# Performance work log

Hardware: AMD Instinct MI355X
Metric: run time of the kernel (lower is better)

The kernel has to match this reference:

```python
import jax, jax.numpy as jnp
import numpy as np

B, N = 32, 256
PHI1, PHI2 = 64, 128
RHO1, RHO2, OUT = 256, 128, 64


def setup_inputs() -> dict:
    key = jax.random.key(0)
    ks = jax.random.split(key, 12)
    dm = jax.random.normal(ks[0], (B, N, N), dtype=jnp.float32)
    lengths = jnp.clip(jax.random.randint(ks[1], (B,), 0, N), 2, N).astype(jnp.int32)

    def lin(k, fan_in, fan_out):
        # torch nn.Linear default init: U(-1/sqrt(fan_in), 1/sqrt(fan_in))
        bound = 1.0 / np.sqrt(fan_in)
        kw, kb = jax.random.split(k)
        W = jax.random.uniform(kw, (fan_in, fan_out), jnp.float32, -bound, bound)
        b = jax.random.uniform(kb, (fan_out,), jnp.float32, -bound, bound)
        return W, b

    W1, b1 = lin(ks[2], 1, PHI1)
    W2, b2 = lin(ks[3], PHI1, PHI2)
    W3, b3 = lin(ks[4], PHI2, RHO1)
    W4, b4 = lin(ks[5], RHO1, RHO2)
    W5, b5 = lin(ks[6], RHO2, OUT)
    return {"dm": dm, "lengths": lengths, "W1": W1, "b1": b1, "W2": W2, "b2": b2,
            "W3": W3, "b3": b3, "W4": W4, "b4": b4, "W5": W5, "b5": b5}


def reference(dm, lengths, W1, b1, W2, b2, W3, b3, W4, b4, W5, b5):
    # Static upper-triangular (offset=1) index pairs: P = N*(N-1)/2
    iu0, iu1 = jnp.triu_indices(N, k=1)
    scalars = dm[:, iu0, iu1]                                   # [B, P]
    # Ragged mask: a pair (i, j) exists only if both indices < item length
    mask = (iu0[None, :] < lengths[:, None]) & (iu1[None, :] < lengths[:, None])  # [B, P]
    # phi MLP applied per scalar: 1 -> 64 -> 128, ReLU after each
    h = jax.nn.relu(scalars[..., None] * W1[0] + b1)            # [B, P, 64]
    h = jax.nn.relu(jnp.einsum('bpd,de->bpe', h, W2) + b2)      # [B, P, 128]
    # Masked sum-pool over pairs
    pooled = jnp.sum(h * mask[..., None].astype(h.dtype), axis=1)  # [B, 128]
    # rho MLP: 128 -> 256 -> 128 -> OUT (ReLU on hidden layers only)
    r = jax.nn.relu(pooled @ W3 + b3)
    r = jax.nn.relu(r @ W4 + b4)
    return r @ W5 + b5                                           # [B, OUT]
```

## Files before the change

### kernel.cpp

```cpp
#include <hip/hip_runtime.h>
#include <hip/hip_bf16.h>


#define NB 32
#define NN 256
#define PHI2 128
#define SEGS 65

__global__ __launch_bounds__(128) void build_tables(
    const float* __restrict__ W1, const float* __restrict__ b1,
    const float* __restrict__ W2, const float* __restrict__ b2,
    float2* __restrict__ table2,
    float* __restrict__ tsort, float* __restrict__ pooled) {
  __shared__ float w2_s[64 * PHI2];
  __shared__ float t_s[64], w1_s[64], b1_s[64];
  __shared__ int cat_s[64], rank_s[64];
  const int tid = threadIdx.x;
  const int seg = blockIdx.x;
  const float4* W2v = (const float4*)W2;
  float4* w2v = (float4*)w2_s;
  for (int i = tid; i < 64 * PHI2 / 4; i += 128) w2v[i] = W2v[i];
  if (tid < 64) {
    float w = W1[tid], bb = b1[tid];
    w1_s[tid] = w; b1_s[tid] = bb;
    int cat; float t;
    if (w > 0.f)      { cat = 0; t = -bb / w; }
    else if (w < 0.f) { cat = 1; t = -bb / w; }
    else              { cat = (bb > 0.f) ? 2 : 3; t = 0.f; }
    t_s[tid] = t; cat_s[tid] = cat;
  }
  __syncthreads();
  if (tid < 64) {
    float t = t_s[tid]; int r = 0;
    for (int k = 0; k < 64; ++k) {
      float tk = t_s[k];
      r += (tk < t) || (tk == t && k < tid);
    }
    rank_s[tid] = r;
    if (seg == 0) tsort[r] = t;
  }
  __syncthreads();
  float a = 0.f, bsum = b2[tid];
#pragma unroll 8
  for (int j = 0; j < 64; ++j) {
    int cat = cat_s[j], r = rank_s[j];
    bool act = (cat == 0) ? (seg > r) : (cat == 1) ? (seg <= r) : (cat == 2);
    float w2 = w2_s[j * PHI2 + tid];
    float m = act ? 1.f : 0.f;
    a    = fmaf(m * w1_s[j], w2, a);
    bsum = fmaf(m * b1_s[j], w2, bsum);
  }
  const int h = tid >> 6, l = tid & 63;
  table2[((h * SEGS) + seg) * 64 + l] = make_float2(a, bsum);
  if (seg == 0) {
    for (int i = tid; i < NB * PHI2; i += 128) pooled[i] = 0.f;
  }
}

__device__ __forceinline__ void visit(float comp, int L, float tv, int lane,
                                      const float2* ab_s, float& acc) {
  float s = __int_as_float(__builtin_amdgcn_readlane(__float_as_int(comp), L));
  int pos = (int)__popcll(__ballot(tv < s));
  float2 p = ab_s[pos * 64 + lane];
  acc += fmaxf(fmaf(p.x, s, p.y), 0.f);
}

__device__ __forceinline__ void visit_dyn(const float4& f4, int j, float tv,
                                          int lane, const float2* ab_s,
                                          float& acc) {
  int c = j & 3;
  float comp = (c == 0) ? f4.x : (c == 1) ? f4.y : (c == 2) ? f4.z : f4.w;
  visit(comp, j >> 2, tv, lane, ab_s, acc);
}

__device__ __forceinline__ void do_row(const float4& f4, int i0, int len,
                                       float tv, int lane,
                                       const float2* ab_s, float& acc) {
  const int jlo = i0 + 1, jhi = len - 1;
  const int fullLo = (jlo + 3) >> 2;
  const int fullHi = (jhi >= 3) ? ((jhi - 3) >> 2) : -1;
  if (fullLo > fullHi) {
    for (int j = jlo; j <= jhi; ++j) visit_dyn(f4, j, tv, lane, ab_s, acc);
    return;
  }
  for (int j = jlo; j < fullLo * 4; ++j) visit_dyn(f4, j, tv, lane, ab_s, acc);
#pragma unroll 4
  for (int L = fullLo; L <= fullHi; ++L) {
    visit(f4.x, L, tv, lane, ab_s, acc);
    visit(f4.y, L, tv, lane, ab_s, acc);
    visit(f4.z, L, tv, lane, ab_s, acc);
    visit(f4.w, L, tv, lane, ab_s, acc);
  }
  for (int j = fullHi * 4 + 4; j <= jhi; ++j)
    visit_dyn(f4, j, tv, lane, ab_s, acc);
}

__global__ __launch_bounds__(512, 8) void phi_pool(
    const float* __restrict__ dm, const int* __restrict__ lengths,
    const float2* __restrict__ table2, const float* __restrict__ tsort,
    float* __restrict__ pooled) {
  __shared__ float2 ab_s[SEGS * 64];
  const int chunk = blockIdx.x;
  const int h     = blockIdx.y;
  const int b     = blockIdx.z;
  const int tid = threadIdx.x;
  const int lane = tid & 63, w = tid >> 6;

  const int len = lengths[b];
  if (8 * chunk > len - 2 && 247 - 8 * chunk > len - 2) return;

  const float2* tg = table2 + h * SEGS * 64;
  for (int i = tid; i < SEGS * 64; i += 512) ab_s[i] = tg[i];
  __syncthreads();

  const float tv = tsort[lane];
  const float* dmb = dm + (size_t)b * (NN * NN);
  float acc = 0.f;

  const int rA = chunk * 8 + w;
  const int rB = 254 - rA;
  const float4 fA = ((const float4*)(dmb + rA * NN))[lane];
  const float4 fB = ((const float4*)(dmb + rB * NN))[lane];
  if (rA <= len - 2) do_row(fA, rA, len, tv, lane, ab_s, acc);
  if (rB != rA && rB <= len - 2) do_row(fB, rB, len, tv, lane, ab_s, acc);

  atomicAdd(&pooled[b * PHI2 + h * 64 + lane], acc);
}

__global__ __launch_bounds__(256) void rho_mlp(
    const float* __restrict__ pooled,
    const float* __restrict__ W3, const float* __restrict__ b3,
    const float* __restrict__ W4, const float* __restrict__ b4,
    const float* __restrict__ W5, const float* __restrict__ b5,
    float* __restrict__ out) {
  __shared__ float w_s[128 * 256];
  __shared__ float p_s[128], r1_s[256], r2_s[128];
  const int b = blockIdx.x, tid = threadIdx.x;
  float4* wsv = (float4*)w_s;
  {
    const float4* w3v = (const float4*)W3;
    for (int i = tid; i < 8192; i += 256) wsv[i] = w3v[i];
  }
  if (tid < 128) p_s[tid] = pooled[b * 128 + tid];
  __syncthreads();
  {
    float acc = b3[tid];
#pragma unroll 8
    for (int k = 0; k < 128; ++k) acc = fmaf(p_s[k], w_s[k * 256 + tid], acc);
    r1_s[tid] = fmaxf(acc, 0.f);
  }
  __syncthreads();
  {
    const float4* w4v = (const float4*)W4;
    for (int i = tid; i < 8192; i += 256) wsv[i] = w4v[i];
  }
  __syncthreads();
  if (tid < 128) {
    float acc = b4[tid];
#pragma unroll 8
    for (int k = 0; k < 256; ++k) acc = fmaf(r1_s[k], w_s[k * 128 + tid], acc);
    r2_s[tid] = fmaxf(acc, 0.f);
  }
  __syncthreads();
  {
    const float4* w5v = (const float4*)W5;
    for (int i = tid; i < 2048; i += 256) wsv[i] = w5v[i];
  }
  __syncthreads();
  if (tid < 64) {
    float acc = b5[tid];
#pragma unroll 8
    for (int k = 0; k < 128; ++k) acc = fmaf(r2_s[k], w_s[k * 64 + tid], acc);
    out[b * 64 + tid] = acc;
  }
}

extern "C" void kernel_launch(void* const* d_in, const int* in_sizes, int n_in,
                              void* d_out, int out_size, void* d_ws, size_t ws_size,
                              hipStream_t stream) {
  const float* dm      = (const float*)d_in[0];
  const int*   lengths = (const int*)d_in[1];
  const float* W1 = (const float*)d_in[2];
  const float* b1 = (const float*)d_in[3];
  const float* W2 = (const float*)d_in[4];
  const float* b2 = (const float*)d_in[5];
  const float* W3 = (const float*)d_in[6];
  const float* b3 = (const float*)d_in[7];
  const float* W4 = (const float*)d_in[8];
  const float* b4 = (const float*)d_in[9];
  const float* W5 = (const float*)d_in[10];
  const float* b5 = (const float*)d_in[11];

  float* ws = (float*)d_ws;
  float2* table2 = (float2*)ws;
  float* tsort   = ws + 16640;
  float* pooled  = ws + 16704;

  build_tables<<<SEGS, 128, 0, stream>>>(W1, b1, W2, b2, table2, tsort, pooled);
  phi_pool<<<dim3(16, 2, NB), 512, 0, stream>>>(dm, lengths, table2, tsort, pooled);
  rho_mlp<<<NB, 256, 0, stream>>>(pooled, W3, b3, W4, b4, W5, b5, (float*)d_out);
}
```

Before: 139.2 us.

## Merge phi halves per block and fuse rho MLP via last-block counter

The table is interleaved so each lane loads a float4 holding the segment coefficients for both 64-channel halves. One block now processes both halves, which halves the dm row reads and the ballot/popcount work per pair. The rho MLP is folded into the phi kernel: a per-batch atomic counter picks the last finishing block, and that block runs the three dense layers reading the weights straight from global memory. This removes one kernel launch, at the cost of doubled shared memory for the table (lower occupancy bound) and a serial tail in the last block.

Result: slower. 161.9 us (+16.3%).

```diff
diff --git a/kernel.cpp b/kernel.cpp
--- a/kernel.cpp
+++ b/kernel.cpp
@@ -1,5 +1,4 @@
 #include <hip/hip_runtime.h>
-#include <hip/hip_bf16.h>
 
 
 #define NB 32
@@ -11,7 +10,8 @@
     const float* __restrict__ W1, const float* __restrict__ b1,
     const float* __restrict__ W2, const float* __restrict__ b2,
     float2* __restrict__ table2,
-    float* __restrict__ tsort, float* __restrict__ pooled) {
+    float* __restrict__ tsort, float* __restrict__ pooled,
+    int* __restrict__ cnt) {
   __shared__ float w2_s[64 * PHI2];
   __shared__ float t_s[64], w1_s[64], b1_s[64];
   __shared__ int cat_s[64], rank_s[64];
@@ -51,126 +51,122 @@
     bsum = fmaf(m * b1_s[j], w2, bsum);
   }
   const int h = tid >> 6, l = tid & 63;
-  table2[((h * SEGS) + seg) * 64 + l] = make_float2(a, bsum);
+  table2[(seg * 64 + l) * 2 + h] = make_float2(a, bsum);
   if (seg == 0) {
     for (int i = tid; i < NB * PHI2; i += 128) pooled[i] = 0.f;
+    if (tid < NB) cnt[tid] = 0;
   }
 }
 
 __device__ __forceinline__ void visit(float comp, int L, float tv, int lane,
-                                      const float2* ab_s, float& acc) {
+                                      const float4* ab_s,
+                                      float& a0, float& a1) {
   float s = __int_as_float(__builtin_amdgcn_readlane(__float_as_int(comp), L));
   int pos = (int)__popcll(__ballot(tv < s));
-  float2 p = ab_s[pos * 64 + lane];
-  acc += fmaxf(fmaf(p.x, s, p.y), 0.f);
+  float4 p = ab_s[pos * 64 + lane];
+  a0 += fmaxf(fmaf(p.x, s, p.y), 0.f);
+  a1 += fmaxf(fmaf(p.z, s, p.w), 0.f);
 }
 
 __device__ __forceinline__ void visit_dyn(const float4& f4, int j, float tv,
-                                          int lane, const float2* ab_s,
-                                          float& acc) {
+                                          int lane, const float4* ab_s,
+                                          float& a0, float& a1) {
   int c = j & 3;
   float comp = (c == 0) ? f4.x : (c == 1) ? f4.y : (c == 2) ? f4.z : f4.w;
-  visit(comp, j >> 2, tv, lane, ab_s, acc);
+  visit(comp, j >> 2, tv, lane, ab_s, a0, a1);
 }
 
 __device__ __forceinline__ void do_row(const float4& f4, int i0, int len,
                                        float tv, int lane,
-                                       const float2* ab_s, float& acc) {
+                                       const float4* ab_s,
+                                       float& a0, float& a1) {
   const int jlo = i0 + 1, jhi = len - 1;
   const int fullLo = (jlo + 3) >> 2;
   const int fullHi = (jhi >= 3) ? ((jhi - 3) >> 2) : -1;
   if (fullLo > fullHi) {
-    for (int j = jlo; j <= jhi; ++j) visit_dyn(f4, j, tv, lane, ab_s, acc);
+    for (int j = jlo; j <= jhi; ++j) visit_dyn(f4, j, tv, lane, ab_s, a0, a1);
     return;
   }
-  for (int j = jlo; j < fullLo * 4; ++j) visit_dyn(f4, j, tv, lane, ab_s, acc);
+  for (int j = jlo; j < fullLo * 4; ++j)
+    visit_dyn(f4, j, tv, lane, ab_s, a0, a1);
 #pragma unroll 4
   for (int L = fullLo; L <= fullHi; ++L) {
-    visit(f4.x, L, tv, lane, ab_s, acc);
-    visit(f4.y, L, tv, lane, ab_s, acc);
-    visit(f4.z, L, tv, lane, ab_s, acc);
-    visit(f4.w, L, tv, lane, ab_s, acc);
+    visit(f4.x, L, tv, lane, ab_s, a0, a1);
+    visit(f4.y, L, tv, lane, ab_s, a0, a1);
+    visit(f4.z, L, tv, lane, ab_s, a0, a1);
+    visit(f4.w, L, tv, lane, ab_s, a0, a1);
   }
   for (int j = fullHi * 4 + 4; j <= jhi; ++j)
-    visit_dyn(f4, j, tv, lane, ab_s, acc);
-}
-
-__global__ __launch_bounds__(512, 8) void phi_pool(
+    visit_dyn(f4, j, tv, lane, ab_s, a0, a1);
+}
+
+__global__ __launch_bounds__(512, 4) void phi_pool_rho(
     const float* __restrict__ dm, const int* __restrict__ lengths,
-    const float2* __restrict__ table2, const float* __restrict__ tsort,
-    float* __restrict__ pooled) {
-  __shared__ float2 ab_s[SEGS * 64];
+    const float4* __restrict__ table4, const float* __restrict__ tsort,
+    float* __restrict__ pooled, int* __restrict__ cnt,
+    const float* __restrict__ W3, const float* __restrict__ b3,
+    const float* __restrict__ W4, const float* __restrict__ b4,
+    const float* __restrict__ W5, const float* __restrict__ b5,
+    float* __restrict__ out) {
+  __shared__ float4 ab_s[SEGS * 64];
+  __shared__ float p_s[128], r1_s[256], r2_s[128];
+  __shared__ int lastflag;
   const int chunk = blockIdx.x;
-  const int h     = blockIdx.y;
-  const int b     = blockIdx.z;
+  const int b     = blockIdx.y;
   const int tid = threadIdx.x;
   const int lane = tid & 63, w = tid >> 6;
 
   const int len = lengths[b];
   if (8 * chunk > len - 2 && 247 - 8 * chunk > len - 2) return;
 
-  const float2* tg = table2 + h * SEGS * 64;
-  for (int i = tid; i < SEGS * 64; i += 512) ab_s[i] = tg[i];
+  for (int i = tid; i < SEGS * 64; i += 512) ab_s[i] = table4[i];
   __syncthreads();
 
   const float tv = tsort[lane];
   const float* dmb = dm + (size_t)b * (NN * NN);
-  float acc = 0.f;
+  float acc0 = 0.f, acc1 = 0.f;
 
   const int rA = chunk * 8 + w;
   const int rB = 254 - rA;
   const float4 fA = ((const float4*)(dmb + rA * NN))[lane];
   const float4 fB = ((const float4*)(dmb + rB * NN))[lane];
-  if (rA <= len - 2) do_row(fA, rA, len, tv, lane, ab_s, acc);
-  if (rB != rA && rB <= len - 2) do_row(fB, rB, len, tv, lane, ab_s, acc);
-
-  atomicAdd(&pooled[b * PHI2 + h * 64 + lane], acc);
-}
-
-__global__ __launch_bounds__(256) void rho_mlp(
-    const float* __restrict__ pooled,
-    const float* __restrict__ W3, const float* __restrict__ b3,
-    const float* __restrict__ W4, const float* __restrict__ b4,
-    const float* __restrict__ W5, const float* __restrict__ b5,
-    float* __restrict__ out) {
-  __shared__ float w_s[128 * 256];
-  __shared__ float p_s[128], r1_s[256], r2_s[128];
-  const int b = blockIdx.x, tid = threadIdx.x;
-  float4* wsv = (float4*)w_s;
-  {
-    const float4* w3v = (const float4*)W3;
-    for (int i = tid; i < 8192; i += 256) wsv[i] = w3v[i];
-  }
-  if (tid < 128) p_s[tid] = pooled[b * 128 + tid];
-  __syncthreads();
-  {
+  if (rA <= len - 2) do_row(fA, rA, len, tv, lane, ab_s, acc0, acc1);
+  if (rB != rA && rB <= len - 2) do_row(fB, rB, len, tv, lane, ab_s, acc0, acc1);
+
+  atomicAdd(&pooled[b * PHI2 + lane], acc0);
+  atomicAdd(&pooled[b * PHI2 + 64 + lane], acc1);
+
+  __threadfence();
+  __syncthreads();
+  if (tid == 0) {
+    int npart = 0;
+    for (int c = 0; c < 16; ++c)
+      npart += (8 * c <= len - 2) || (247 - 8 * c <= len - 2);
+    lastflag = (atomicAdd(&cnt[b], 1) == npart - 1) ? 1 : 0;
+  }
+  __syncthreads();
+  if (!lastflag) return;
+
+  if (tid < 128) p_s[tid] = atomicAdd(&pooled[b * PHI2 + tid], 0.0f);
+  __syncthreads();
+  if (tid < 256) {
     float acc = b3[tid];
 #pragma unroll 8
-    for (int k = 0; k < 128; ++k) acc = fmaf(p_s[k], w_s[k * 256 + tid], acc);
+    for (int k = 0; k < 128; ++k) acc = fmaf(p_s[k], W3[k * 256 + tid], acc);
     r1_s[tid] = fmaxf(acc, 0.f);
-  }
-  __syncthreads();
-  {
-    const float4* w4v = (const float4*)W4;
-    for (int i = tid; i < 8192; i += 256) wsv[i] = w4v[i];
   }
   __syncthreads();
   if (tid < 128) {
     float acc = b4[tid];
 #pragma unroll 8
-    for (int k = 0; k < 256; ++k) acc = fmaf(r1_s[k], w_s[k * 128 + tid], acc);
+    for (int k = 0; k < 256; ++k) acc = fmaf(r1_s[k], W4[k * 128 + tid], acc);
     r2_s[tid] = fmaxf(acc, 0.f);
-  }
-  __syncthreads();
-  {
-    const float4* w5v = (const float4*)W5;
-    for (int i = tid; i < 2048; i += 256) wsv[i] = w5v[i];
   }
   __syncthreads();
   if (tid < 64) {
     float acc = b5[tid];
 #pragma unroll 8
-    for (int k = 0; k < 128; ++k) acc = fmaf(r2_s[k], w_s[k * 64 + tid], acc);
+    for (int k = 0; k < 128; ++k) acc = fmaf(r2_s[k], W5[k * 64 + tid], acc);
     out[b * 64 + tid] = acc;
   }
 }
@@ -192,11 +188,14 @@
   const float* b5 = (const float*)d_in[11];
 
   float* ws = (float*)d_ws;
-  float2* table2 = (float2*)ws;
+  float4* table4 = (float4*)ws;
   float* tsort   = ws + 16640;
   float* pooled  = ws + 16704;
-
-  build_tables<<<SEGS, 128, 0, stream>>>(W1, b1, W2, b2, table2, tsort, pooled);
-  phi_pool<<<dim3(16, 2, NB), 512, 0, stream>>>(dm, lengths, table2, tsort, pooled);
-  rho_mlp<<<NB, 256, 0, stream>>>(pooled, W3, b3, W4, b4, W5, b5, (float*)d_out);
-}
+  int*   cnt     = (int*)(ws + 20800);
+
+  build_tables<<<SEGS, 128, 0, stream>>>(W1, b1, W2, b2, (float2*)table4,
+                                         tsort, pooled, cnt);
+  phi_pool_rho<<<dim3(16, NB), 512, 0, stream>>>(
+      dm, lengths, table4, tsort, pooled, cnt,
+      W3, b3, W4, b4, W5, b5, (float*)d_out);
+}
```

## Fuse rho MLP into phi pooling kernel via last-block atomic counter

Applied to the files above, without the earlier changes.

Removes the separate rho_mlp launch. Each phi_pool block bumps a per-batch counter after its atomic accumulation, and the last block for that batch element runs the three rho layers, reading weights straight from global memory instead of staging them in shared memory. The inner pair loop is also restructured to issue four broadcasts, ballots and table loads before the accumulations, to expose more instruction-level parallelism, with the unroll dropped from 4 to 2. This saves a kernel launch and its gap, but adds a threadfence and a serial tail MLP done by one block per batch element, and the partition count must match the early-exit condition exactly.

Result: slower. 216.9 us (+55.8%).

```diff
diff --git a/kernel.cpp b/kernel.cpp
--- a/kernel.cpp
+++ b/kernel.cpp
@@ -1,5 +1,4 @@
 #include <hip/hip_runtime.h>
-#include <hip/hip_bf16.h>
 
 
 #define NB 32
@@ -11,7 +10,8 @@
     const float* __restrict__ W1, const float* __restrict__ b1,
     const float* __restrict__ W2, const float* __restrict__ b2,
     float2* __restrict__ table2,
-    float* __restrict__ tsort, float* __restrict__ pooled) {
+    float* __restrict__ tsort, float* __restrict__ pooled,
+    int* __restrict__ cnt) {
   __shared__ float w2_s[64 * PHI2];
   __shared__ float t_s[64], w1_s[64], b1_s[64];
   __shared__ int cat_s[64], rank_s[64];
@@ -54,14 +54,21 @@
   table2[((h * SEGS) + seg) * 64 + l] = make_float2(a, bsum);
   if (seg == 0) {
     for (int i = tid; i < NB * PHI2; i += 128) pooled[i] = 0.f;
-  }
+    if (tid < NB) cnt[tid] = 0;
+  }
+}
+
+__device__ __forceinline__ float bcast(float v, int L) {
+  return __int_as_float(__builtin_amdgcn_readlane(__float_as_int(v), L));
+}
+__device__ __forceinline__ int segof(float tv, float s) {
+  return (int)__popcll(__ballot(tv < s));
 }
 
 __device__ __forceinline__ void visit(float comp, int L, float tv, int lane,
                                       const float2* ab_s, float& acc) {
-  float s = __int_as_float(__builtin_amdgcn_readlane(__float_as_int(comp), L));
-  int pos = (int)__popcll(__ballot(tv < s));
-  float2 p = ab_s[pos * 64 + lane];
+  float s = bcast(comp, L);
+  float2 p = ab_s[segof(tv, s) * 64 + lane];
   acc += fmaxf(fmaf(p.x, s, p.y), 0.f);
 }
 
@@ -84,22 +91,36 @@
     return;
   }
   for (int j = jlo; j < fullLo * 4; ++j) visit_dyn(f4, j, tv, lane, ab_s, acc);
-#pragma unroll 4
+#pragma unroll 2
   for (int L = fullLo; L <= fullHi; ++L) {
-    visit(f4.x, L, tv, lane, ab_s, acc);
-    visit(f4.y, L, tv, lane, ab_s, acc);
-    visit(f4.z, L, tv, lane, ab_s, acc);
-    visit(f4.w, L, tv, lane, ab_s, acc);
+    float s0 = bcast(f4.x, L), s1 = bcast(f4.y, L);
+    float s2 = bcast(f4.z, L), s3 = bcast(f4.w, L);
+    int p0 = segof(tv, s0), p1 = segof(tv, s1);
+    int p2 = segof(tv, s2), p3 = segof(tv, s3);
+    float2 q0 = ab_s[p0 * 64 + lane];
+    float2 q1 = ab_s[p1 * 64 + lane];
+    float2 q2 = ab_s[p2 * 64 + lane];
+    float2 q3 = ab_s[p3 * 64 + lane];
+    acc += fmaxf(fmaf(q0.x, s0, q0.y), 0.f);
+    acc += fmaxf(fmaf(q1.x, s1, q1.y), 0.f);
+    acc += fmaxf(fmaf(q2.x, s2, q2.y), 0.f);
+    acc += fmaxf(fmaf(q3.x, s3, q3.y), 0.f);
   }
   for (int j = fullHi * 4 + 4; j <= jhi; ++j)
     visit_dyn(f4, j, tv, lane, ab_s, acc);
 }
 
-__global__ __launch_bounds__(512, 8) void phi_pool(
+__global__ __launch_bounds__(512, 8) void phi_pool_rho(
     const float* __restrict__ dm, const int* __restrict__ lengths,
     const float2* __restrict__ table2, const float* __restrict__ tsort,
-    float* __restrict__ pooled) {
+    float* __restrict__ pooled, int* __restrict__ cnt,
+    const float* __restrict__ W3, const float* __restrict__ b3,
+    const float* __restrict__ W4, const float* __restrict__ b4,
+    const float* __restrict__ W5, const float* __restrict__ b5,
+    float* __restrict__ out) {
   __shared__ float2 ab_s[SEGS * 64];
+  __shared__ float p_s[128], r1_s[256], r2_s[128];
+  __shared__ int lastflag;
   const int chunk = blockIdx.x;
   const int h     = blockIdx.y;
   const int b     = blockIdx.z;
@@ -125,53 +146,40 @@
   if (rB != rA && rB <= len - 2) do_row(fB, rB, len, tv, lane, ab_s, acc);
 
   atomicAdd(&pooled[b * PHI2 + h * 64 + lane], acc);
-}
-
-__global__ __launch_bounds__(256) void rho_mlp(
-    const float* __restrict__ pooled,
-    const float* __restrict__ W3, const float* __restrict__ b3,
-    const float* __restrict__ W4, const float* __restrict__ b4,
-    const float* __restrict__ W5, const float* __restrict__ b5,
-    float* __restrict__ out) {
-  __shared__ float w_s[128 * 256];
-  __shared__ float p_s[128], r1_s[256], r2_s[128];
-  const int b = blockIdx.x, tid = threadIdx.x;
-  float4* wsv = (float4*)w_s;
-  {
-    const float4* w3v = (const float4*)W3;
-    for (int i = tid; i < 8192; i += 256) wsv[i] = w3v[i];
-  }
-  if (tid < 128) p_s[tid] = pooled[b * 128 + tid];
-  __syncthreads();
-  {
-    float acc = b3[tid];
-#pragma unroll 8
-    for (int k = 0; k < 128; ++k) acc = fmaf(p_s[k], w_s[k * 256 + tid], acc);
-    r1_s[tid] = fmaxf(acc, 0.f);
-  }
-  __syncthreads();
-  {
-    const float4* w4v = (const float4*)W4;
-    for (int i = tid; i < 8192; i += 256) wsv[i] = w4v[i];
+
+  __threadfence();
+  __syncthreads();
+  if (tid == 0) {
+    int npart = 0;
+    for (int c = 0; c < 16; ++c)
+      npart += (8 * c <= len - 2) || (247 - 8 * c <= len - 2);
+    npart *= 2;
+    lastflag = (atomicAdd(&cnt[b], 1) == npart - 1) ? 1 : 0;
+  }
+  __syncthreads();
+  if (!lastflag) return;
+
+  if (tid < 128) p_s[tid] = atomicAdd(&pooled[b * PHI2 + tid], 0.0f);
+  __syncthreads();
+  if (tid < 256) {
+    float acc2 = b3[tid];
+#pragma unroll 8
+    for (int k = 0; k < 128; ++k) acc2 = fmaf(p_s[k], W3[k * 256 + tid], acc2);
+    r1_s[tid] = fmaxf(acc2, 0.f);
   }
   __syncthreads();
   if (tid < 128) {
-    float acc = b4[tid];
-#pragma unroll 8
-    for (int k = 0; k < 256; ++k) acc = fmaf(r1_s[k], w_s[k * 128 + tid], acc);
-    r2_s[tid] = fmaxf(acc, 0.f);
-  }
-  __syncthreads();
-  {
-    const float4* w5v = (const float4*)W5;
-    for (int i = tid; i < 2048; i += 256) wsv[i] = w5v[i];
+    float acc2 = b4[tid];
+#pragma unroll 8
+    for (int k = 0; k < 256; ++k) acc2 = fmaf(r1_s[k], W4[k * 128 + tid], acc2);
+    r2_s[tid] = fmaxf(acc2, 0.f);
   }
   __syncthreads();
   if (tid < 64) {
-    float acc = b5[tid];
-#pragma unroll 8
-    for (int k = 0; k < 128; ++k) acc = fmaf(r2_s[k], w_s[k * 64 + tid], acc);
-    out[b * 64 + tid] = acc;
+    float acc2 = b5[tid];
+#pragma unroll 8
+    for (int k = 0; k < 128; ++k) acc2 = fmaf(r2_s[k], W5[k * 64 + tid], acc2);
+    out[b * 64 + tid] = acc2;
   }
 }
 
@@ -195,8 +203,11 @@
   float2* table2 = (float2*)ws;
   float* tsort   = ws + 16640;
   float* pooled  = ws + 16704;
-
-  build_tables<<<SEGS, 128, 0, stream>>>(W1, b1, W2, b2, table2, tsort, pooled);
-  phi_pool<<<dim3(16, 2, NB), 512, 0, stream>>>(dm, lengths, table2, tsort, pooled);
-  rho_mlp<<<NB, 256, 0, stream>>>(pooled, W3, b3, W4, b4, W5, b5, (float*)d_out);
-}
+  int*   cnt     = (int*)(ws + 20800);
+
+  build_tables<<<SEGS, 128, 0, stream>>>(W1, b1, W2, b2, table2, tsort,
+                                         pooled, cnt);
+  phi_pool_rho<<<dim3(16, 2, NB), 512, 0, stream>>>(
+      dm, lengths, table2, tsort, pooled, cnt,
+      W3, b3, W4, b4, W5, b5, (float*)d_out);
+}
```
